# Performance work log

Measured on AMD Instinct MI355X. Metric: run time of the kernel, lower is better.

Reference implementation:

```python
import jax, jax.numpy as jnp
import numpy as np

B, CIN, COUT, H, W_ = 8, 16, 16, 1024, 1024
KH = KW = 3
PH = PW = 1


def setup_inputs() -> dict:
    key = jax.random.key(0)
    kx, kw = jax.random.split(key)
    x = jax.random.normal(kx, (B, CIN, H, W_), dtype=jnp.float32)
    # Conv weight, OIHW layout, no bias (bias=False in source)
    Wt = jax.random.normal(kw, (COUT, CIN, KH, KW), dtype=jnp.float32) * 0.1
    return {"x": x, "W": Wt}


def reference(x, W):
    # The original forward splits the input into nTh x nTw = 16 tiles, runs
    # conv2d_1 per tile with halo padding, and stitches tile outputs into a
    # preallocated buffer. Mathematically this equals a single 3x3, stride-1,
    # pad-1 convolution over the full input (same padding, bias=False).
    return jax.lax.conv_general_dilated(
        x, W,
        window_strides=(1, 1),
        padding=((PH, PH), (PW, PW)),
        dimension_numbers=("NCHW", "OIHW", "NCHW"),
    )
```

## Files before the change

### kernel.cpp

```cpp
#include <hip/hip_runtime.h>


typedef _Float16 f16x4 __attribute__((ext_vector_type(4)));
typedef _Float16 f16x2 __attribute__((ext_vector_type(2)));
typedef float f32x4 __attribute__((ext_vector_type(4)));

#define B_N    8
#define C_IN   16
#define C_OUT  16
#define H_N    1024
#define W_N    1024
#define TILE_W 64
#define TILE_H 16
#define LDS_R  (TILE_H + 2)
#define LDS_W  (TILE_W + 2)
#define CPAD   20

__global__ __launch_bounds__(256, 3) void conv3x3_mfma(
    const float* __restrict__ x, const float* __restrict__ wt,
    float* __restrict__ out)
{
    __shared__ _Float16 s_x[LDS_R][LDS_W][CPAD];

    const int w0   = blockIdx.x * TILE_W;
    const int h0   = blockIdx.y * TILE_H;
    const int b    = blockIdx.z;
    const int tid  = threadIdx.x;
    const int lane = tid & 63;
    const int q    = lane >> 4;
    const int ln   = lane & 15;
    const int wave = tid >> 6;
    const int seg  = wave * 16;

#pragma unroll
    for (int it = 0; it < 9; ++it) {
        const int flat = tid + 256 * it;
        const int i4 = flat & 15;
        const int cp = (flat >> 4) & 7;
        const int r  = flat >> 7;
        const int gh = h0 - 1 + r;
        const int gw = w0 + 4 * i4;
        f32x4 va = {0.f, 0.f, 0.f, 0.f};
        f32x4 vb = {0.f, 0.f, 0.f, 0.f};
        if ((unsigned)gh < (unsigned)H_N) {
            const size_t base =
                (((size_t)b * C_IN + 2 * cp) * H_N + gh) * W_N + gw;
            va = *(const f32x4*)&x[base];
            vb = *(const f32x4*)&x[base + (size_t)H_N * W_N];
        }
#pragma unroll
        for (int j = 0; j < 4; ++j) {
            f16x2 p;
            p[0] = (_Float16)va[j];
            p[1] = (_Float16)vb[j];
            *(f16x2*)&s_x[r][1 + 4 * i4 + j][2 * cp] = p;
        }
    }

#pragma unroll
    for (int it = 0; it < 2; ++it) {
        const int f2 = tid + 256 * it;
        if (f2 < 288) {
            const int side = f2 & 1;
            const int cp   = (f2 >> 1) & 7;
            const int r    = f2 >> 4;
            const int i    = side ? (LDS_W - 1) : 0;
            const int gw   = w0 - 1 + i;
            const int gh   = h0 - 1 + r;
            float a = 0.f, c2 = 0.f;
            if ((unsigned)gh < (unsigned)H_N && (unsigned)gw < (unsigned)W_N) {
                const size_t base =
                    (((size_t)b * C_IN + 2 * cp) * H_N + gh) * W_N + gw;
                a  = x[base];
                c2 = x[base + (size_t)H_N * W_N];
            }
            f16x2 p;
            p[0] = (_Float16)a;
            p[1] = (_Float16)c2;
            *(f16x2*)&s_x[r][i][2 * cp] = p;
        }
    }

    f16x4 bfrag[9];
#pragma unroll
    for (int kh = 0; kh < 3; ++kh) {
#pragma unroll
        for (int kw = 0; kw < 3; ++kw) {
            f16x4 f;
#pragma unroll
            for (int j = 0; j < 4; ++j) {
                const int cin = 4 * q + j;
                f[j] = (_Float16)wt[((ln * C_IN + cin) * 3 + kh) * 3 + kw];
            }
            bfrag[kh * 3 + kw] = f;
        }
    }

    __syncthreads();

    f32x4 acc[3];
    const size_t outbase = ((size_t)b * C_OUT + ln) * H_N;
#pragma unroll
    for (int ir = 0; ir < LDS_R; ++ir) {
        const f16x4 a0 = *(const f16x4*)&s_x[ir][seg + ln + 0][4 * q];
        const f16x4 a1 = *(const f16x4*)&s_x[ir][seg + ln + 1][4 * q];
        const f16x4 a2 = *(const f16x4*)&s_x[ir][seg + ln + 2][4 * q];

        if (ir <= TILE_H - 1) {
            f32x4 t = {0.f, 0.f, 0.f, 0.f};
            t = __builtin_amdgcn_mfma_f32_16x16x16f16(a0, bfrag[0], t, 0, 0, 0);
            t = __builtin_amdgcn_mfma_f32_16x16x16f16(a1, bfrag[1], t, 0, 0, 0);
            t = __builtin_amdgcn_mfma_f32_16x16x16f16(a2, bfrag[2], t, 0, 0, 0);
            acc[ir % 3] = t;
        }
        if (ir >= 1 && ir - 1 <= TILE_H - 1) {
            f32x4 t = acc[(ir - 1) % 3];
            t = __builtin_amdgcn_mfma_f32_16x16x16f16(a0, bfrag[3], t, 0, 0, 0);
            t = __builtin_amdgcn_mfma_f32_16x16x16f16(a1, bfrag[4], t, 0, 0, 0);
            t = __builtin_amdgcn_mfma_f32_16x16x16f16(a2, bfrag[5], t, 0, 0, 0);
            acc[(ir - 1) % 3] = t;
        }
        if (ir >= 2) {
            const int r = ir - 2;
            f32x4 t = acc[r % 3];
            t = __builtin_amdgcn_mfma_f32_16x16x16f16(a0, bfrag[6], t, 0, 0, 0);
            t = __builtin_amdgcn_mfma_f32_16x16x16f16(a1, bfrag[7], t, 0, 0, 0);
            t = __builtin_amdgcn_mfma_f32_16x16x16f16(a2, bfrag[8], t, 0, 0, 0);
            const int wout = w0 + seg + 4 * q;
            *(f32x4*)&out[(outbase + (h0 + r)) * W_N + wout] = t;
        }
    }
}

extern "C" void kernel_launch(void* const* d_in, const int* in_sizes, int n_in,
                              void* d_out, int out_size, void* d_ws, size_t ws_size,
                              hipStream_t stream) {
    const float* x  = (const float*)d_in[0];
    const float* wt = (const float*)d_in[1];
    float* out = (float*)d_out;
    dim3 grid(W_N / TILE_W, H_N / TILE_H, B_N);
    conv3x3_mfma<<<grid, 256, 0, stream>>>(x, wt, out);
}
```

Measured before the change: 957.9 us.

## Swizzle LDS channel layout and halve tile height for higher occupancy

New measurement: 968.1 us. Within noise of the previous version (+1.1%).

```diff
diff --git a/kernel.cpp b/kernel.cpp
--- a/kernel.cpp
+++ b/kernel.cpp
@@ -11,16 +11,15 @@
 #define H_N    1024
 #define W_N    1024
 #define TILE_W 64
-#define TILE_H 16
+#define TILE_H 8
 #define LDS_R  (TILE_H + 2)
 #define LDS_W  (TILE_W + 2)
-#define CPAD   20
 
-__global__ __launch_bounds__(256, 3) void conv3x3_mfma(
+__global__ __launch_bounds__(256, 6) void conv3x3_mfma(
     const float* __restrict__ x, const float* __restrict__ wt,
     float* __restrict__ out)
 {
-    __shared__ _Float16 s_x[LDS_R][LDS_W][CPAD];
+    __shared__ _Float16 s_x[LDS_R * LDS_W * 16];
 
     const int w0   = blockIdx.x * TILE_W;
     const int h0   = blockIdx.y * TILE_H;
@@ -33,7 +32,7 @@
     const int seg  = wave * 16;
 
 #pragma unroll
-    for (int it = 0; it < 9; ++it) {
+    for (int it = 0; it < 5; ++it) {
         const int flat = tid + 256 * it;
         const int i4 = flat & 15;
         const int cp = (flat >> 4) & 7;
@@ -50,35 +49,34 @@
         }
 #pragma unroll
         for (int j = 0; j < 4; ++j) {
+            const int px = 1 + 4 * i4 + j;
+            const int su = (cp >> 1) ^ ((px >> 2) & 3);
             f16x2 p;
             p[0] = (_Float16)va[j];
             p[1] = (_Float16)vb[j];
-            *(f16x2*)&s_x[r][1 + 4 * i4 + j][2 * cp] = p;
+            *(f16x2*)&s_x[(r * LDS_W + px) * 16 + su * 4 + 2 * (cp & 1)] = p;
         }
     }
 
-#pragma unroll
-    for (int it = 0; it < 2; ++it) {
-        const int f2 = tid + 256 * it;
-        if (f2 < 288) {
-            const int side = f2 & 1;
-            const int cp   = (f2 >> 1) & 7;
-            const int r    = f2 >> 4;
-            const int i    = side ? (LDS_W - 1) : 0;
-            const int gw   = w0 - 1 + i;
-            const int gh   = h0 - 1 + r;
-            float a = 0.f, c2 = 0.f;
-            if ((unsigned)gh < (unsigned)H_N && (unsigned)gw < (unsigned)W_N) {
-                const size_t base =
-                    (((size_t)b * C_IN + 2 * cp) * H_N + gh) * W_N + gw;
-                a  = x[base];
-                c2 = x[base + (size_t)H_N * W_N];
-            }
-            f16x2 p;
-            p[0] = (_Float16)a;
-            p[1] = (_Float16)c2;
-            *(f16x2*)&s_x[r][i][2 * cp] = p;
+    if (tid < 160) {
+        const int side = tid & 1;
+        const int cp   = (tid >> 1) & 7;
+        const int r    = tid >> 4;
+        const int px   = side ? (LDS_W - 1) : 0;
+        const int gw   = w0 - 1 + px;
+        const int gh   = h0 - 1 + r;
+        float a = 0.f, c2 = 0.f;
+        if ((unsigned)gh < (unsigned)H_N && (unsigned)gw < (unsigned)W_N) {
+            const size_t base =
+                (((size_t)b * C_IN + 2 * cp) * H_N + gh) * W_N + gw;
+            a  = x[base];
+            c2 = x[base + (size_t)H_N * W_N];
         }
+        const int su = (cp >> 1) ^ ((px >> 2) & 3);
+        f16x2 p;
+        p[0] = (_Float16)a;
+        p[1] = (_Float16)c2;
+        *(f16x2*)&s_x[(r * LDS_W + px) * 16 + su * 4 + 2 * (cp & 1)] = p;
     }
 
     f16x4 bfrag[9];
@@ -102,9 +100,13 @@
     const size_t outbase = ((size_t)b * C_OUT + ln) * H_N;
 #pragma unroll
     for (int ir = 0; ir < LDS_R; ++ir) {
-        const f16x4 a0 = *(const f16x4*)&s_x[ir][seg + ln + 0][4 * q];
-        const f16x4 a1 = *(const f16x4*)&s_x[ir][seg + ln + 1][4 * q];
-        const f16x4 a2 = *(const f16x4*)&s_x[ir][seg + ln + 2][4 * q];
+        const int pxb = seg + ln;
+        const int sw0 = (q ^ (((pxb + 0) >> 2) & 3)) << 2;
+        const int sw1 = (q ^ (((pxb + 1) >> 2) & 3)) << 2;
+        const int sw2 = (q ^ (((pxb + 2) >> 2) & 3)) << 2;
+        const f16x4 a0 = *(const f16x4*)&s_x[(ir * LDS_W + pxb + 0) * 16 + sw0];
+        const f16x4 a1 = *(const f16x4*)&s_x[(ir * LDS_W + pxb + 1) * 16 + sw1];
+        const f16x4 a2 = *(const f16x4*)&s_x[(ir * LDS_W + pxb + 2) * 16 + sw2];
 
         if (ir <= TILE_H - 1) {
             f32x4 t = {0.f, 0.f, 0.f, 0.f};
```
